# Optimization experiments

Hardware: AMD Instinct MI355X
Metric: run time of the kernel (lower is better)

## Reference

```python
import jax, jax.numpy as jnp
import numpy as np

N_NODES = 1_000_000
D_FEAT = 128
N_QUERY = 100_000
NUM_SAMPLE = 10


def setup_inputs() -> dict:
    key = jax.random.key(0)
    k1, k2 = jax.random.split(key)
    features = jax.random.normal(k1, (N_NODES, D_FEAT), dtype=jnp.float32)
    # pre-sampled neighbor ids per query node (replaces neighbour_sample's RNG)
    nbrs = jax.random.randint(k2, (N_QUERY, NUM_SAMPLE), 0, N_NODES)
    return {"features": features, "nbrs": nbrs, "num_sample": NUM_SAMPLE}


def reference(features, nbrs, num_sample):
    # ragged neighbor gather + per-node max-pool, fused into one vectorized op
    gathered = features[nbrs]              # [B, S, d]
    return jnp.max(gathered, axis=1)       # [B, d]
```

## Files before the change

kernel.cpp:

```cpp
#include <hip/hip_runtime.h>


typedef __attribute__((ext_vector_type(4))) float f32x4;

template <int S>
__global__ __launch_bounds__(256) void maxpool_s(
    const float* __restrict__ feats,
    const int* __restrict__ nbrs,
    float* __restrict__ out,
    int n_query)
{
    int idx = blockIdx.x * blockDim.x + threadIdx.x;
    int q = idx >> 5;
    int g = idx & 31;
    if (q >= n_query) return;

    const long base = (long)q * S;

    f32x4 m;
    {
        int nbr = nbrs[base];
        m = *((const f32x4*)(feats + (size_t)nbr * 128) + g);
    }
    #pragma unroll
    for (int s = 1; s < S; ++s) {
        int nbr = nbrs[base + s];
        f32x4 v = *((const f32x4*)(feats + (size_t)nbr * 128) + g);
        m[0] = fmaxf(m[0], v[0]);
        m[1] = fmaxf(m[1], v[1]);
        m[2] = fmaxf(m[2], v[2]);
        m[3] = fmaxf(m[3], v[3]);
    }

    *((f32x4*)(out + (size_t)q * 128) + g) = m;
}

__global__ __launch_bounds__(256) void maxpool_generic(
    const float* __restrict__ feats,
    const int* __restrict__ nbrs,
    float* __restrict__ out,
    int n_query, int num_sample)
{
    int idx = blockIdx.x * blockDim.x + threadIdx.x;
    int q = idx >> 5;
    int g = idx & 31;
    if (q >= n_query) return;

    const long base = (long)q * num_sample;

    f32x4 m;
    {
        int nbr = nbrs[base];
        m = *((const f32x4*)(feats + (size_t)nbr * 128) + g);
    }
    for (int s = 1; s < num_sample; ++s) {
        int nbr = nbrs[base + s];
        f32x4 v = *((const f32x4*)(feats + (size_t)nbr * 128) + g);
        m[0] = fmaxf(m[0], v[0]);
        m[1] = fmaxf(m[1], v[1]);
        m[2] = fmaxf(m[2], v[2]);
        m[3] = fmaxf(m[3], v[3]);
    }

    *((f32x4*)(out + (size_t)q * 128) + g) = m;
}

extern "C" void kernel_launch(void* const* d_in, const int* in_sizes, int n_in,
                              void* d_out, int out_size, void* d_ws, size_t ws_size,
                              hipStream_t stream) {
    const float* feats = (const float*)d_in[0];
    const int*   nbrs  = (const int*)d_in[1];
    float*       out   = (float*)d_out;

    const int D = 128;
    int n_query = out_size / D;
    int num_sample = (n_query > 0) ? (in_sizes[1] / n_query) : 1;

    int total = n_query * 32;
    int blocks = (total + 255) / 256;

    if (num_sample == 10) {
        maxpool_s<10><<<blocks, 256, 0, stream>>>(feats, nbrs, out, n_query);
    } else {
        maxpool_generic<<<blocks, 256, 0, stream>>>(feats, nbrs, out, n_query, num_sample);
    }
}
```

Measured before the change: 640.8 us.

## Map one wavefront per query with scalar neighbor indices and float2 loads

Each query is now handled by a full 64-lane wavefront instead of 32 lanes, with each lane loading a float2 instead of a float4. The neighbor ids are loaded once and made wave-uniform with readfirstlane, so address generation can run on the scalar unit rather than through per-lane index loads. Output uses nontemporal stores to avoid polluting cache. The risk is that half-width loads issue twice as many memory instructions per byte, and the total thread count doubles for a gather-bound workload.

```diff
diff --git a/kernel.cpp b/kernel.cpp
--- a/kernel.cpp
+++ b/kernel.cpp
@@ -1,38 +1,39 @@
 #include <hip/hip_runtime.h>
 
 
-typedef __attribute__((ext_vector_type(4))) float f32x4;
+typedef __attribute__((ext_vector_type(2))) float f32x2;
 
 template <int S>
-__global__ __launch_bounds__(256) void maxpool_s(
+__global__ __launch_bounds__(256) void maxpool_wave(
     const float* __restrict__ feats,
     const int* __restrict__ nbrs,
     float* __restrict__ out,
     int n_query)
 {
-    int idx = blockIdx.x * blockDim.x + threadIdx.x;
-    int q = idx >> 5;
-    int g = idx & 31;
-    if (q >= n_query) return;
+    const int wave = blockIdx.x * (blockDim.x >> 6) + (threadIdx.x >> 6);
+    const int lane = threadIdx.x & 63;
+    if (wave >= n_query) return;
 
-    const long base = (long)q * S;
+    const int q = __builtin_amdgcn_readfirstlane(wave);
 
-    f32x4 m;
-    {
-        int nbr = nbrs[base];
-        m = *((const f32x4*)(feats + (size_t)nbr * 128) + g);
-    }
+    const int* np = nbrs + (size_t)q * S;
+    int idxs[S];
+    #pragma unroll
+    for (int s = 0; s < S; ++s)
+        idxs[s] = __builtin_amdgcn_readfirstlane(np[s]);
+
+    const f32x2* fcol = (const f32x2*)feats + lane;
+
+    f32x2 m = fcol[(size_t)idxs[0] * 64];
     #pragma unroll
     for (int s = 1; s < S; ++s) {
-        int nbr = nbrs[base + s];
-        f32x4 v = *((const f32x4*)(feats + (size_t)nbr * 128) + g);
-        m[0] = fmaxf(m[0], v[0]);
-        m[1] = fmaxf(m[1], v[1]);
-        m[2] = fmaxf(m[2], v[2]);
-        m[3] = fmaxf(m[3], v[3]);
+        f32x2 v = fcol[(size_t)idxs[s] * 64];
+        m.x = fmaxf(m.x, v.x);
+        m.y = fmaxf(m.y, v.y);
     }
 
-    *((f32x4*)(out + (size_t)q * 128) + g) = m;
+    f32x2* op = (f32x2*)out + (size_t)q * 64 + lane;
+    __builtin_nontemporal_store(m, op);
 }
 
 __global__ __launch_bounds__(256) void maxpool_generic(
@@ -41,28 +42,23 @@
     float* __restrict__ out,
     int n_query, int num_sample)
 {
-    int idx = blockIdx.x * blockDim.x + threadIdx.x;
-    int q = idx >> 5;
-    int g = idx & 31;
-    if (q >= n_query) return;
+    const int wave = blockIdx.x * (blockDim.x >> 6) + (threadIdx.x >> 6);
+    const int lane = threadIdx.x & 63;
+    if (wave >= n_query) return;
 
-    const long base = (long)q * num_sample;
+    const int q = __builtin_amdgcn_readfirstlane(wave);
+    const int* np = nbrs + (size_t)q * num_sample;
+    const f32x2* fcol = (const f32x2*)feats + lane;
 
-    f32x4 m;
-    {
-        int nbr = nbrs[base];
-        m = *((const f32x4*)(feats + (size_t)nbr * 128) + g);
+    f32x2 m = fcol[(size_t)__builtin_amdgcn_readfirstlane(np[0]) * 64];
+    for (int s = 1; s < num_sample; ++s) {
+        int nbr = __builtin_amdgcn_readfirstlane(np[s]);
+        f32x2 v = fcol[(size_t)nbr * 64];
+        m.x = fmaxf(m.x, v.x);
+        m.y = fmaxf(m.y, v.y);
     }
-    for (int s = 1; s < num_sample; ++s) {
-        int nbr = nbrs[base + s];
-        f32x4 v = *((const f32x4*)(feats + (size_t)nbr * 128) + g);
-        m[0] = fmaxf(m[0], v[0]);
-        m[1] = fmaxf(m[1], v[1]);
-        m[2] = fmaxf(m[2], v[2]);
-        m[3] = fmaxf(m[3], v[3]);
-    }
-
-    *((f32x4*)(out + (size_t)q * 128) + g) = m;
+    f32x2* op = (f32x2*)out + (size_t)q * 64 + lane;
+    __builtin_nontemporal_store(m, op);
 }
 
 extern "C" void kernel_launch(void* const* d_in, const int* in_sizes, int n_in,
@@ -76,11 +72,11 @@
     int n_query = out_size / D;
     int num_sample = (n_query > 0) ? (in_sizes[1] / n_query) : 1;
 
-    int total = n_query * 32;
-    int blocks = (total + 255) / 256;
+    const int waves_per_block = 4;
+    int blocks = (n_query + waves_per_block - 1) / waves_per_block;
 
     if (num_sample == 10) {
-        maxpool_s<10><<<blocks, 256, 0, stream>>>(feats, nbrs, out, n_query);
+        maxpool_wave<10><<<blocks, 256, 0, stream>>>(feats, nbrs, out, n_query);
     } else {
         maxpool_generic<<<blocks, 256, 0, stream>>>(feats, nbrs, out, n_query, num_sample);
     }
```

Result: no change. 643.0 us (+0.3%).
